# Performance work log

Hardware: AMD Instinct MI355X
Metric: run time of the kernel (lower is better)

## Reference

```python
import jax, jax.numpy as jnp
import numpy as np
from jax import lax

jax.config.update("jax_enable_x64", True)  # needed for the int64 fixed-point requant

B, H_IN, W_IN, CIN = 64, 226, 226, 32
KH, KW = 3, 3
H_OUT, W_OUT = H_IN - KH + 1, W_IN - KW + 1  # valid conv: 224x224


def setup_inputs() -> dict:
    key = jax.random.key(0)
    k1, k2, k3 = jax.random.split(key, 3)
    inp = jax.random.randint(k1, (B, H_IN, W_IN, CIN), -128, 128, dtype=jnp.int32)
    flt = jax.random.randint(k2, (B, KH, KW, CIN), -128, 128, dtype=jnp.int32)
    bias = jax.random.randint(k3, (B,), -1000, 1000, dtype=jnp.int32)
    return {
        "input": inp,
        "filt": flt,
        "bias": bias,
        "q_mantissa": 1518500250,  # ~0.7071 * 2^31, typical TFLite requant mantissa
        "exponent": -3,
        "output_zero_point": -5,
    }


def _multiply_by_quantize_mul(x_i64, q_mantissa: int, exponent: int):
    # Faithful to the source (note Python precedence: (q_mantissa + (1<<15)) >> 16)
    if q_mantissa < 2147418112:
        reduced_mantissa = (q_mantissa + (1 << 15)) >> 16
    else:
        reduced_mantissa = 32767
    total_shifts = 15 - exponent
    x = x_i64 * jnp.int64(reduced_mantissa)
    x = x + jnp.int64(1 << (total_shifts - 1))
    return x >> total_shifts  # arithmetic right shift, rounding-half-up


def reference(input, filt, bias, q_mantissa, exponent, output_zero_point):
    # Per-slice valid correlation with int32 accumulation:
    # acc[i,j,k] = sum_{m,n,o} input[i,j+m,k+n,o] * filt[i,m,n,o]
    def one_slice(x, w):
        # x: (H_IN, W_IN, CIN) int32, w: (KH, KW, CIN) int32 -> (H_OUT, W_OUT, 1)
        return lax.conv_general_dilated(
            x[None], w[..., None],  # NHWC, HWIO (Cout=1)
            window_strides=(1, 1), padding="VALID",
            dimension_numbers=("NHWC", "HWIO", "NHWC"),
            preferred_element_type=jnp.int32,
        )[0]

    acc = jax.vmap(one_slice)(input, filt)            # (B, H_OUT, W_OUT, 1) int32
    acc = acc + bias[:, None, None, None]             # int32 bias add
    acc = _multiply_by_quantize_mul(acc.astype(jnp.int64), int(q_mantissa), int(exponent))
    acc = acc + jnp.int64(output_zero_point)
    acc = jnp.clip(acc, -128, 127)
    return acc.astype(jnp.int8)                        # (B, H_OUT, W_OUT, 1)
```

## Files before the change

kernel.cpp:

```cpp
#include <hip/hip_runtime.h>


typedef int int4v __attribute__((ext_vector_type(4)));
typedef int int2v __attribute__((ext_vector_type(2)));

#define B_       64
#define H_IN_    226
#define W_IN_    226
#define CIN_     32
#define H_OUT_   224
#define W_OUT_   224
#define ROWP     (W_IN_ * CIN_)
#define IMGP     (H_IN_ * ROWP)
#define HB       28
#define MAXREL   (HB + 1)

#define LOADROW(slot, r) {                                              \
    int rr_ = (r); if (rr_ > MAXREL) rr_ = MAXREL;                      \
    const int* p_ = base + rr_ * ROWP;                                  \
    x[slot][0] = *(const int4v*)(p_);                                   \
    x[slot][1] = *(const int4v*)(p_ + CIN_);                            \
    x[slot][2] = *(const int4v*)(p_ + 2 * CIN_);                        \
    x[slot][3] = *(const int4v*)(p_ + 3 * CIN_);                        \
}

#define ACCUM(sm, m)                                                    \
    _Pragma("unroll")                                                   \
    for (int n = 0; n < 3; ++n) {                                       \
        _Pragma("unroll")                                               \
        for (int c = 0; c < 4; ++c) {                                   \
            a0 += __mul24(x[sm][n][c],     f[m][n][c]);                 \
            a1 += __mul24(x[sm][n + 1][c], f[m][n][c]);                 \
        }                                                               \
    }

#define BODY(s0, s1, s2, hh) {                                          \
    int a0 = 0, a1 = 0;                                                 \
    ACCUM(s0, 0) ACCUM(s1, 1) ACCUM(s2, 2)                              \
    a0 += __shfl_xor(a0, 1); a0 += __shfl_xor(a0, 2); a0 += __shfl_xor(a0, 4); \
    a1 += __shfl_xor(a1, 1); a1 += __shfl_xor(a1, 2); a1 += __shfl_xor(a1, 4); \
    if (ci == 0) {                                                      \
        long long v0 = (((long long)(a0 + bi)) * rm + rnd) >> ts;       \
        long long v1 = (((long long)(a1 + bi)) * rm + rnd) >> ts;       \
        int i0 = (int)v0 + zp, i1 = (int)v1 + zp;                       \
        i0 = min(127, max(-128, i0));                                   \
        i1 = min(127, max(-128, i1));                                   \
        int2v r_; r_[0] = i0; r_[1] = i1;                               \
        *reinterpret_cast<int2v*>(ob + (hh) * W_OUT_) = r_;             \
    }                                                                   \
}

__global__ __launch_bounds__(256) void conv2d_requant_kernel(
    const int* __restrict__ in,
    const int* __restrict__ filt,
    const int* __restrict__ bias,
    const int* __restrict__ qm_p,
    const int* __restrict__ ex_p,
    const int* __restrict__ zp_p,
    int* __restrict__ out)
{
    const int bx   = blockIdx.x;
    const int b    = bx / 28;
    const int seg  = bx % 28;
    const int widx = seg * 4 + (threadIdx.x >> 6);
    const int strip = widx / 14;
    const int wseg  = widx % 14;
    const int h0 = strip * HB;
    const int w0 = wseg * 16;
    const int lane = threadIdx.x & 63;
    const int wi = lane >> 3;
    const int ci = lane & 7;

    const int qm = qm_p[0];
    const int ex = ex_p[0];
    const int zp = zp_p[0];
    const int rm = (qm < 2147418112) ? ((qm + (1 << 15)) >> 16) : 32767;
    const int ts = 15 - ex;
    const long long rnd = 1LL << (ts - 1);
    const int bi = bias[b];

    int f[3][3][4];
    {
        const int* fb = filt + b * 288 + ci * 4;
#pragma unroll
        for (int m = 0; m < 3; ++m) {
#pragma unroll
            for (int n = 0; n < 3; ++n) {
                int4v t = *(const int4v*)(fb + (m * 3 + n) * CIN_);
                f[m][n][0] = t[0]; f[m][n][1] = t[1];
                f[m][n][2] = t[2]; f[m][n][3] = t[3];
            }
        }
    }

    const int* base = in + b * IMGP + h0 * ROWP + (w0 + 2 * wi) * CIN_ + ci * 4;
    int* ob = out + (b * H_OUT_ + h0) * W_OUT_ + w0 + 2 * wi;

    int4v x[4][4];
    LOADROW(0, 0)
    LOADROW(1, 1)
    LOADROW(2, 2)

    for (int hh = 0; hh < HB; hh += 4) {
        LOADROW(3, hh + 3) BODY(0, 1, 2, hh)
        LOADROW(0, hh + 4) BODY(1, 2, 3, hh + 1)
        LOADROW(1, hh + 5) BODY(2, 3, 0, hh + 2)
        LOADROW(2, hh + 6) BODY(3, 0, 1, hh + 3)
    }
}

extern "C" void kernel_launch(void* const* d_in, const int* in_sizes, int n_in,
                              void* d_out, int out_size, void* d_ws, size_t ws_size,
                              hipStream_t stream) {
    const int* in   = (const int*)d_in[0];
    const int* filt = (const int*)d_in[1];
    const int* bias = (const int*)d_in[2];
    const int* qm   = (const int*)d_in[3];
    const int* ex   = (const int*)d_in[4];
    const int* zp   = (const int*)d_in[5];
    int* out = (int*)d_out;

    dim3 grid(B_ * 28);
    dim3 block(256);
    hipLaunchKernelGGL(conv2d_requant_kernel, grid, block, 0, stream,
                       in, filt, bias, qm, ex, zp, out);
}
```

Before: 91.76 us.

## Pack int8 values into words and use sdot4 dot products

Input and filter values, which fit in int8, are packed four per 32-bit register and accumulated with the sdot4 builtin. This replaces twelve mul24 multiply-adds per filter tap with one dot instruction per packed word. Loads are now issued one row ahead of the packing step, which keeps fewer raw registers live and deepens the prefetch. Launch bounds also request four blocks per CU. Packing costs extra ALU work for every loaded row, and the kernel is likely bound by memory bandwidth on the int32 input, so the compute savings may be partly hidden.

```diff
diff --git a/kernel.cpp b/kernel.cpp
--- a/kernel.cpp
+++ b/kernel.cpp
@@ -15,28 +15,48 @@
 #define HB       28
 #define MAXREL   (HB + 1)
 
-#define LOADROW(slot, r) {                                              \
-    int rr_ = (r); if (rr_ > MAXREL) rr_ = MAXREL;                      \
-    const int* p_ = base + rr_ * ROWP;                                  \
-    x[slot][0] = *(const int4v*)(p_);                                   \
-    x[slot][1] = *(const int4v*)(p_ + CIN_);                            \
-    x[slot][2] = *(const int4v*)(p_ + 2 * CIN_);                        \
-    x[slot][3] = *(const int4v*)(p_ + 3 * CIN_);                        \
+__device__ __forceinline__ int pack4(int a, int b, int c, int d) {
+    return (a & 0xff) | ((b & 0xff) << 8) | ((c & 0xff) << 16) | (d << 24);
 }
 
-#define ACCUM(sm, m)                                                    \
-    _Pragma("unroll")                                                   \
-    for (int n = 0; n < 3; ++n) {                                       \
-        _Pragma("unroll")                                               \
-        for (int c = 0; c < 4; ++c) {                                   \
-            a0 += __mul24(x[sm][n][c],     f[m][n][c]);                 \
-            a1 += __mul24(x[sm][n + 1][c], f[m][n][c]);                 \
-        }                                                               \
-    }
+__device__ __forceinline__ int dot4(int a, int b, int c) {
+#if __has_builtin(__builtin_amdgcn_sdot4)
+    return __builtin_amdgcn_sdot4(a, b, c, false);
+#else
+    return c + ((a << 24) >> 24) * ((b << 24) >> 24)
+             + ((a << 16) >> 24) * ((b << 16) >> 24)
+             + ((a << 8)  >> 24) * ((b << 8)  >> 24)
+             + ( a        >> 24) * ( b        >> 24);
+#endif
+}
+
+#define LOADRAW(row) {                                                  \
+    int rr_ = (row); if (rr_ > MAXREL) rr_ = MAXREL;                    \
+    const int* p_ = base + rr_ * ROWP;                                  \
+    r[0] = *(const int4v*)(p_);                                         \
+    r[1] = *(const int4v*)(p_ + CIN_);                                  \
+    r[2] = *(const int4v*)(p_ + 2 * CIN_);                              \
+    r[3] = *(const int4v*)(p_ + 3 * CIN_);                              \
+}
+
+#define PACK(slot) {                                                    \
+    P[slot][0] = pack4(r[0][0], r[0][1], r[0][2], r[0][3]);             \
+    P[slot][1] = pack4(r[1][0], r[1][1], r[1][2], r[1][3]);             \
+    P[slot][2] = pack4(r[2][0], r[2][1], r[2][2], r[2][3]);             \
+    P[slot][3] = pack4(r[3][0], r[3][1], r[3][2], r[3][3]);             \
+}
 
 #define BODY(s0, s1, s2, hh) {                                          \
     int a0 = 0, a1 = 0;                                                 \
-    ACCUM(s0, 0) ACCUM(s1, 1) ACCUM(s2, 2)                              \
+    _Pragma("unroll")                                                   \
+    for (int n = 0; n < 3; ++n) {                                       \
+        a0 = dot4(P[s0][n],     F[0][n], a0);                           \
+        a1 = dot4(P[s0][n + 1], F[0][n], a1);                           \
+        a0 = dot4(P[s1][n],     F[1][n], a0);                           \
+        a1 = dot4(P[s1][n + 1], F[1][n], a1);                           \
+        a0 = dot4(P[s2][n],     F[2][n], a0);                           \
+        a1 = dot4(P[s2][n + 1], F[2][n], a1);                           \
+    }                                                                   \
     a0 += __shfl_xor(a0, 1); a0 += __shfl_xor(a0, 2); a0 += __shfl_xor(a0, 4); \
     a1 += __shfl_xor(a1, 1); a1 += __shfl_xor(a1, 2); a1 += __shfl_xor(a1, 4); \
     if (ci == 0) {                                                      \
@@ -45,12 +65,14 @@
         int i0 = (int)v0 + zp, i1 = (int)v1 + zp;                       \
         i0 = min(127, max(-128, i0));                                   \
         i1 = min(127, max(-128, i1));                                   \
-        int2v r_; r_[0] = i0; r_[1] = i1;                               \
-        *reinterpret_cast<int2v*>(ob + (hh) * W_OUT_) = r_;             \
+        int2v o_; o_[0] = i0; o_[1] = i1;                               \
+        *reinterpret_cast<int2v*>(ob + (hh) * W_OUT_) = o_;             \
     }                                                                   \
 }
 
-__global__ __launch_bounds__(256) void conv2d_requant_kernel(
+#define STEP(sp, s0, s1, s2, hh, nr)  PACK(sp) LOADRAW(nr) BODY(s0, s1, s2, hh)
+
+__global__ __launch_bounds__(256, 4) void conv2d_requant_kernel(
     const int* __restrict__ in,
     const int* __restrict__ filt,
     const int* __restrict__ bias,
@@ -79,7 +101,7 @@
     const long long rnd = 1LL << (ts - 1);
     const int bi = bias[b];
 
-    int f[3][3][4];
+    int F[3][3];
     {
         const int* fb = filt + b * 288 + ci * 4;
 #pragma unroll
@@ -87,8 +109,7 @@
 #pragma unroll
             for (int n = 0; n < 3; ++n) {
                 int4v t = *(const int4v*)(fb + (m * 3 + n) * CIN_);
-                f[m][n][0] = t[0]; f[m][n][1] = t[1];
-                f[m][n][2] = t[2]; f[m][n][3] = t[3];
+                F[m][n] = pack4(t[0], t[1], t[2], t[3]);
             }
         }
     }
@@ -96,16 +117,18 @@
     const int* base = in + b * IMGP + h0 * ROWP + (w0 + 2 * wi) * CIN_ + ci * 4;
     int* ob = out + (b * H_OUT_ + h0) * W_OUT_ + w0 + 2 * wi;
 
-    int4v x[4][4];
-    LOADROW(0, 0)
-    LOADROW(1, 1)
-    LOADROW(2, 2)
+    int P[4][4];
+    int4v r[4];
+    LOADRAW(0) PACK(0)
+    LOADRAW(1) PACK(1)
+    LOADRAW(2) PACK(2)
+    LOADRAW(3)
 
     for (int hh = 0; hh < HB; hh += 4) {
-        LOADROW(3, hh + 3) BODY(0, 1, 2, hh)
-        LOADROW(0, hh + 4) BODY(1, 2, 3, hh + 1)
-        LOADROW(1, hh + 5) BODY(2, 3, 0, hh + 2)
-        LOADROW(2, hh + 6) BODY(3, 0, 1, hh + 3)
+        STEP(3, 0, 1, 2, hh,     hh + 4)
+        STEP(0, 1, 2, 3, hh + 1, hh + 5)
+        STEP(1, 2, 3, 0, hh + 2, hh + 6)
+        STEP(2, 3, 0, 1, hh + 3, hh + 7)
     }
 }
 
```

New measurement: 88.42 us (median of 2 runs). -3.6%, faster.
